# Performance work log

Measured on AMD Instinct MI355X. Metric: run time of the kernel, lower is better.

The kernel has to match this reference:

```python
import jax, jax.numpy as jnp
import numpy as np

BATCH, DIM, HEADS = 512, 2048, 16
CPH = DIM // HEADS  # per-head channels = 128
EPS = 1e-5


def setup_inputs() -> dict:
    key = jax.random.key(0)
    ks = jax.random.split(key, 6)
    x = jax.random.normal(ks[0], (BATCH, DIM, 1, 1), dtype=jnp.float32)
    W_qv = jax.random.normal(ks[1], (2 * DIM, DIM), dtype=jnp.float32) * (1.0 / np.sqrt(DIM))
    temperature = jnp.ones((HEADS, 1, 1), dtype=jnp.float32)
    k_param = jax.random.normal(ks[2], (BATCH, DIM, 1, 1), dtype=jnp.float32)
    bias_param = jax.random.normal(ks[3], (BATCH, HEADS, CPH * CPH, 1), dtype=jnp.float32)
    bn_gamma = jnp.ones((HEADS,), dtype=jnp.float32)
    bn_beta = jnp.zeros((HEADS,), dtype=jnp.float32)
    W_out = jax.random.normal(ks[4], (DIM, DIM, 1, 1), dtype=jnp.float32) * (1.0 / np.sqrt(DIM))
    b_out = jax.random.normal(ks[5], (DIM,), dtype=jnp.float32) * 0.01
    return {"x": x, "W_qv": W_qv, "temperature": temperature, "k_param": k_param,
            "bias_param": bias_param, "bn_gamma": bn_gamma, "bn_beta": bn_beta,
            "W_out": W_out, "b_out": b_out}


def reference(x, W_qv, temperature, k_param, bias_param, bn_gamma, bn_beta, W_out, b_out):
    b, c, h, w = x.shape  # h = w = 1 (required by x.squeeze() + Linear)
    heads = temperature.shape[0]
    cph = c // heads

    xs = x.reshape(b, c)
    qv = xs @ W_qv.T                     # [b, 2c]
    q, v = qv[:, :c], qv[:, c:]
    q = q.reshape(b, heads, cph, 1)      # b head c (h w)
    v = v.reshape(b, heads, cph, 1)
    k = k_param.reshape(b, heads, cph, 1)

    # BatchNorm2d over channel = head (training-mode batch stats, biased var)
    mean = jnp.mean(v, axis=(0, 2, 3), keepdims=True)
    var = jnp.var(v, axis=(0, 2, 3), keepdims=True)
    v = (v - mean) * jax.lax.rsqrt(var + EPS)
    v = v * bn_gamma.reshape(1, heads, 1, 1) + bn_beta.reshape(1, heads, 1, 1)

    # attn = q @ k^T over the singleton spatial dim -> [b, head, cph, cph]
    attn = jnp.einsum('bhcx,bhdx->bhcd', q, k)
    attn = attn + bias_param.reshape(b, heads, cph, cph)
    attn = attn * temperature  # [heads,1,1] broadcasts over batch
    attn = jax.nn.softmax(attn, axis=-1)

    out = jnp.einsum('bhcd,bhdx->bhcx', attn, v)  # [b, head, cph, 1]
    out = out.reshape(b, c)

    # 1x1 conv == matmul
    out = out @ W_out.reshape(c, c).T + b_out
    return out.reshape(b, c, 1, 1)
```

## Files before the change

### kernel.cpp

```cpp
#include <hip/hip_runtime.h>
#include <hip/hip_bf16.h>
#include <cstdint>

#define NBATCH 512
#define NDIM   2048
#define NHEADS 16
#define NCPH   128

typedef __bf16 bf16x8 __attribute__((ext_vector_type(8)));
typedef float  f32x4  __attribute__((ext_vector_type(4)));

__device__ __forceinline__ unsigned short f2bf(float f) {
    uint32_t u = __builtin_bit_cast(uint32_t, f);
    u += 0x7FFFu + ((u >> 16) & 1u);
    return (unsigned short)(u >> 16);
}

__device__ __forceinline__ void gl_lds16(const void* g, void* l) {
    __builtin_amdgcn_global_load_lds(
        (const __attribute__((address_space(1))) void*)g,
        (__attribute__((address_space(3))) void*)l,
        16, 0, 0);
}

template<int BM, int BN, int BK, bool A_BF16, bool BNP>
__global__ __launch_bounds__(256) void gemm_f(
    const unsigned short* __restrict__ Abf, const float* __restrict__ Af,
    const float* __restrict__ Bf, float* __restrict__ C,
    const float* __restrict__ bias, float* __restrict__ bnpart,
    int M, int N, int K)
{
    constexpr int WM = BM / 2, WN = BN / 2;
    constexpr int MI = WM / 16, NI = WN / 16;
    constexpr int CPR = BK / 8;
    constexpr int RA = (BM * BK) / 8 / 256;
    constexpr int GA = (BM * BK) / 2048;
    constexpr int RB = (BN * BK) / 8 / 256;

    __shared__ unsigned short As[2][BM * BK];
    __shared__ unsigned short Bs[2][BN * BK];

    const int tid  = threadIdx.x;
    const int lane = tid & 63;
    const int wid  = tid >> 6;
    const int wr   = wid >> 1;
    const int wc   = wid & 1;
    const int m0   = blockIdx.y * BM;
    const int n0   = blockIdx.x * BN;
    const int fr   = lane & 15;
    const int kq   = lane >> 4;

    f32x4 acc[MI][NI] = {};
    float4 rga[RA > 0 ? RA : 1][2], rgb[RB][2];

    auto load_A = [&](int bs, int k0) {
        if constexpr (A_BF16) {
#pragma unroll
            for (int r = 0; r < GA; r++) {
                const int e   = r * 2048 + tid * 8;
                const int row = e / BK;
                const int swz = ((((e % BK) >> 3) ^ (row & 7)) << 3);
                gl_lds16(Abf + (size_t)(m0 + row) * K + k0 + swz, &As[bs][e]);
            }
        } else {
#pragma unroll
            for (int r = 0; r < RA; r++) {
                const int idx = r * 256 + tid;
                const int row = idx / CPR, cc = idx % CPR;
                const float4* g = (const float4*)(Af + (size_t)(m0 + row) * K
                                                  + k0 + cc * 8);
                rga[r][0] = g[0];
                rga[r][1] = g[1];
            }
        }
    };
    auto load_B = [&](int k0) {
#pragma unroll
        for (int r = 0; r < RB; r++) {
            const int idx = r * 256 + tid;
            const int row = idx / CPR, cc = idx % CPR;
            const float4* g = (const float4*)(Bf + (size_t)(n0 + row) * K
                                              + k0 + cc * 8);
            rgb[r][0] = g[0];
            rgb[r][1] = g[1];
        }
    };
    auto write_A = [&](int bs) {
        if constexpr (!A_BF16) {
#pragma unroll
            for (int r = 0; r < RA; r++) {
                const int idx = r * 256 + tid;
                const int row = idx / CPR, cc = idx % CPR;
                bf16x8 v;
                v[0] = (__bf16)rga[r][0].x; v[1] = (__bf16)rga[r][0].y;
                v[2] = (__bf16)rga[r][0].z; v[3] = (__bf16)rga[r][0].w;
                v[4] = (__bf16)rga[r][1].x; v[5] = (__bf16)rga[r][1].y;
                v[6] = (__bf16)rga[r][1].z; v[7] = (__bf16)rga[r][1].w;
                *(bf16x8*)&As[bs][row * BK + ((cc ^ (row & 7)) << 3)] = v;
            }
        }
    };
    auto write_B = [&](int bs) {
#pragma unroll
        for (int r = 0; r < RB; r++) {
            const int idx = r * 256 + tid;
            const int row = idx / CPR, cc = idx % CPR;
            bf16x8 v;
            v[0] = (__bf16)rgb[r][0].x; v[1] = (__bf16)rgb[r][0].y;
            v[2] = (__bf16)rgb[r][0].z; v[3] = (__bf16)rgb[r][0].w;
            v[4] = (__bf16)rgb[r][1].x; v[5] = (__bf16)rgb[r][1].y;
            v[6] = (__bf16)rgb[r][1].z; v[7] = (__bf16)rgb[r][1].w;
            *(bf16x8*)&Bs[bs][row * BK + ((cc ^ (row & 7)) << 3)] = v;
        }
    };
    auto compute = [&](int bs) {
#pragma unroll
        for (int kh = 0; kh < BK / 32; kh++) {
            const int kchunk = kh * 4 + kq;
            bf16x8 af[MI], bfv[NI];
#pragma unroll
            for (int i = 0; i < MI; i++) {
                const int row = wr * WM + i * 16 + fr;
                af[i] = *(const bf16x8*)&As[bs][row * BK
                        + ((kchunk ^ (row & 7)) << 3)];
            }
#pragma unroll
            for (int j = 0; j < NI; j++) {
                const int row = wc * WN + j * 16 + fr;
                bfv[j] = *(const bf16x8*)&Bs[bs][row * BK
                         + ((kchunk ^ (row & 7)) << 3)];
            }
#pragma unroll
            for (int i = 0; i < MI; i++)
#pragma unroll
                for (int j = 0; j < NI; j++)
                    acc[i][j] = __builtin_amdgcn_mfma_f32_16x16x32_bf16(
                        af[i], bfv[j], acc[i][j], 0, 0, 0);
        }
    };

    load_A(0, 0);
    load_B(0);
    write_A(0);
    write_B(0);
    __syncthreads();

    const int NT = K / BK;
    int cur = 0;
    for (int t = 0; t < NT - 1; t++) {
        load_A(cur ^ 1, (t + 1) * BK);
        load_B((t + 1) * BK);
        compute(cur);
        write_A(cur ^ 1);
        write_B(cur ^ 1);
        __syncthreads();
        cur ^= 1;
    }
    compute(cur);

    const int row0 = m0 + wr * WM + (kq << 2);
    const int col0 = n0 + wc * WN + fr;
#pragma unroll
    for (int j = 0; j < NI; j++) {
        const int cc = col0 + j * 16;
        const float badd = bias ? bias[cc] : 0.0f;
#pragma unroll
        for (int i = 0; i < MI; i++)
#pragma unroll
            for (int r = 0; r < 4; r++)
                C[(size_t)(row0 + i * 16 + r) * N + cc] = acc[i][j][r] + badd;
    }

    if (BNP && n0 >= NDIM) {
        float s = 0.f, ss = 0.f;
#pragma unroll
        for (int i = 0; i < MI; i++)
#pragma unroll
            for (int j = 0; j < NI; j++)
#pragma unroll
                for (int r = 0; r < 4; r++) {
                    const float v = acc[i][j][r];
                    s += v;
                    ss = fmaf(v, v, ss);
                }
#pragma unroll
        for (int off = 32; off; off >>= 1) {
            s  += __shfl_down(s, off);
            ss += __shfl_down(ss, off);
        }
        __shared__ float rs[4], rss[4];
        if (lane == 0) { rs[wid] = s; rss[wid] = ss; }
        __syncthreads();
        if (tid == 0)
            ((float2*)bnpart)[((n0 - NDIM) >> 6) * 8 + (m0 >> 6)] =
                make_float2(rs[0] + rs[1] + rs[2] + rs[3],
                            rss[0] + rss[1] + rss[2] + rss[3]);
    }
}

__global__ __launch_bounds__(256) void attn_k(
    const float* __restrict__ qv, const float* __restrict__ kparam,
    const float* __restrict__ bias, const float* __restrict__ temperature,
    const float* __restrict__ bnpart, const float* __restrict__ gamma,
    const float* __restrict__ beta, unsigned short* __restrict__ aout)
{
    const int bh = blockIdx.x;
    const int b  = bh >> 4;
    const int h  = bh & 15;
    const int tid = threadIdx.x;

    __shared__ float ks[NCPH], vsr[NCPH], s2sh[2];
    if (tid < 32)
        ((float4*)ks)[tid] =
            ((const float4*)(kparam + (size_t)b * NDIM + h * NCPH))[tid];
    else if (tid < 64)
        ((float4*)vsr)[tid - 32] =
            ((const float4*)(qv + (size_t)b * (2 * NDIM) + NDIM + h * NCPH))[tid - 32];

    if (tid < 16) {
        float2 p = ((const float2*)bnpart)[(h * 2 + (tid >> 3)) * 8 + (tid & 7)];
        float s = p.x, ss = p.y;
#pragma unroll
        for (int off = 8; off; off >>= 1) {
            s  += __shfl_xor(s, off);
            ss += __shfl_xor(ss, off);
        }
        if (tid == 0) {
            const float inv = 1.0f / (NBATCH * NCPH);
            float mean = s * inv;
            float var  = ss * inv - mean * mean;
            float sc   = gamma[h] * rsqrtf(var + 1e-5f);
            s2sh[0] = sc;
            s2sh[1] = beta[h] - mean * sc;
        }
    }

    const int c = tid >> 1, half = tid & 1;
    const float qc   = qv[(size_t)b * (2 * NDIM) + h * NCPH + c];
    const float temp = temperature[h];

    const float4* bp = (const float4*)(bias + ((size_t)bh << 14)
                                       + (size_t)c * NCPH + half * 64);
    float4 l4[16];
#pragma unroll
    for (int j = 0; j < 16; j++) l4[j] = bp[j];

    __syncthreads();
    const float sc = s2sh[0], sh = s2sh[1];
    const float4* kk4 = (const float4*)(ks  + half * 64);
    const float4* vv4 = (const float4*)(vsr + half * 64);

    float s0 = 0.f, s1 = 0.f, o0 = 0.f, o1 = 0.f;
#pragma unroll
    for (int j = 0; j < 16; j++) {
        const float4 bb = l4[j];
        const float4 kx = kk4[j];
        const float4 vx = vv4[j];
        float px = __expf(fmaf(qc, kx.x, bb.x) * temp);
        float py = __expf(fmaf(qc, kx.y, bb.y) * temp);
        float pz = __expf(fmaf(qc, kx.z, bb.z) * temp);
        float pw = __expf(fmaf(qc, kx.w, bb.w) * temp);
        s0 += px; s1 += py; s0 += pz; s1 += pw;
        o0 = fmaf(px, vx.x, o0);
        o1 = fmaf(py, vx.y, o1);
        o0 = fmaf(pz, vx.z, o0);
        o1 = fmaf(pw, vx.w, o1);
    }
    float s = s0 + s1, o = o0 + o1;
    s += __shfl_xor(s, 1);
    o += __shfl_xor(o, 1);

    if (half == 0)
        aout[(size_t)b * NDIM + h * NCPH + c] = f2bf(fmaf(sc, o / s, sh));
}

extern "C" void kernel_launch(void* const* d_in, const int* in_sizes, int n_in,
                              void* d_out, int out_size, void* d_ws, size_t ws_size,
                              hipStream_t stream)
{
    const float* x      = (const float*)d_in[0];
    const float* Wqv    = (const float*)d_in[1];
    const float* temp   = (const float*)d_in[2];
    const float* kparam = (const float*)d_in[3];
    const float* bias   = (const float*)d_in[4];
    const float* gamma  = (const float*)d_in[5];
    const float* beta   = (const float*)d_in[6];
    const float* Wout   = (const float*)d_in[7];
    const float* bout   = (const float*)d_in[8];
    float* out = (float*)d_out;

    char* ws = (char*)d_ws;
    float*          qv     = (float*)(ws);
    unsigned short* ao_bf  = (unsigned short*)(ws + 8388608);
    float*          bnpart = (float*)(ws + 10485760);

    gemm_f<64, 64, 128, false, true><<<dim3(64, 8), 256, 0, stream>>>(
        nullptr, x, Wqv, qv, nullptr, bnpart, NBATCH, 2 * NDIM, NDIM);

    attn_k<<<NBATCH * NHEADS, 256, 0, stream>>>(
        qv, kparam, bias, temp, bnpart, gamma, beta, ao_bf);

    gemm_f<64, 32, 128, true, false><<<dim3(64, 8), 256, 0, stream>>>(
        ao_bf, nullptr, Wout, out, bout, nullptr, NBATCH, NDIM, NDIM);
}
```

Measured before the change: 163.1 us.

## Pre-convert Wqv and x to bf16 and stage both QV GEMM operands via direct-to-LDS loads

Adds a conversion kernel that turns W_qv and x into bf16 in workspace on every call. A new GEMM variant then loads both operands with global_load_lds DMA instead of fp32 register loads followed by conversion and LDS writes. The aim is to cut VGPR staging and conversion work in the QV GEMM main loop and let loads overlap compute more cleanly. The cost is an extra kernel launch that reads 32 MB of fp32 and writes 16 MB of bf16, which may outweigh the savings in the GEMM.

Measured after the change: 163.3 us. No clear change (+0.1%).

```diff
diff --git a/kernel.cpp b/kernel.cpp
--- a/kernel.cpp
+++ b/kernel.cpp
@@ -23,19 +23,32 @@
         16, 0, 0);
 }
 
-template<int BM, int BN, int BK, bool A_BF16, bool BNP>
-__global__ __launch_bounds__(256) void gemm_f(
-    const unsigned short* __restrict__ Abf, const float* __restrict__ Af,
-    const float* __restrict__ Bf, float* __restrict__ C,
-    const float* __restrict__ bias, float* __restrict__ bnpart,
+__global__ __launch_bounds__(256) void cvt_wx(
+    const float* __restrict__ wqv, const float* __restrict__ x,
+    unsigned short* __restrict__ owqv, unsigned short* __restrict__ ox)
+{
+    const int t = blockIdx.x * 256 + threadIdx.x;
+    const int n1 = (2 * NDIM * NDIM) / 4;
+    const float4* src; unsigned short* dst; int idx;
+    if (t < n1) { src = (const float4*)wqv; dst = owqv; idx = t; }
+    else        { src = (const float4*)x;   dst = ox;   idx = t - n1; }
+    float4 v = src[idx];
+    ushort4 o;
+    o.x = f2bf(v.x); o.y = f2bf(v.y); o.z = f2bf(v.z); o.w = f2bf(v.w);
+    *(ushort4*)(dst + (size_t)idx * 4) = o;
+}
+
+template<int BM, int BN, int BK, bool BNP>
+__global__ __launch_bounds__(256) void gemm_dma(
+    const unsigned short* __restrict__ Abf,
+    const unsigned short* __restrict__ Bbf,
+    float* __restrict__ C, float* __restrict__ bnpart,
     int M, int N, int K)
 {
     constexpr int WM = BM / 2, WN = BN / 2;
     constexpr int MI = WM / 16, NI = WN / 16;
-    constexpr int CPR = BK / 8;
-    constexpr int RA = (BM * BK) / 8 / 256;
     constexpr int GA = (BM * BK) / 2048;
-    constexpr int RB = (BN * BK) / 8 / 256;
+    constexpr int GB = (BN * BK) / 2048;
 
     __shared__ unsigned short As[2][BM * BK];
     __shared__ unsigned short Bs[2][BN * BK];
@@ -51,27 +64,136 @@
     const int kq   = lane >> 4;
 
     f32x4 acc[MI][NI] = {};
-    float4 rga[RA > 0 ? RA : 1][2], rgb[RB][2];
+
+    auto stage = [&](int bs, int k0) {
+#pragma unroll
+        for (int r = 0; r < GA; r++) {
+            const int e   = r * 2048 + tid * 8;
+            const int row = e / BK;
+            const int swz = ((((e % BK) >> 3) ^ (row & 7)) << 3);
+            gl_lds16(Abf + (size_t)(m0 + row) * K + k0 + swz, &As[bs][e]);
+        }
+#pragma unroll
+        for (int r = 0; r < GB; r++) {
+            const int e   = r * 2048 + tid * 8;
+            const int row = e / BK;
+            const int swz = ((((e % BK) >> 3) ^ (row & 7)) << 3);
+            gl_lds16(Bbf + (size_t)(n0 + row) * K + k0 + swz, &Bs[bs][e]);
+        }
+    };
+    auto compute = [&](int bs) {
+#pragma unroll
+        for (int kh = 0; kh < BK / 32; kh++) {
+            const int kchunk = kh * 4 + kq;
+            bf16x8 af[MI], bfv[NI];
+#pragma unroll
+            for (int i = 0; i < MI; i++) {
+                const int row = wr * WM + i * 16 + fr;
+                af[i] = *(const bf16x8*)&As[bs][row * BK
+                        + ((kchunk ^ (row & 7)) << 3)];
+            }
+#pragma unroll
+            for (int j = 0; j < NI; j++) {
+                const int row = wc * WN + j * 16 + fr;
+                bfv[j] = *(const bf16x8*)&Bs[bs][row * BK
+                         + ((kchunk ^ (row & 7)) << 3)];
+            }
+#pragma unroll
+            for (int i = 0; i < MI; i++)
+#pragma unroll
+                for (int j = 0; j < NI; j++)
+                    acc[i][j] = __builtin_amdgcn_mfma_f32_16x16x32_bf16(
+                        af[i], bfv[j], acc[i][j], 0, 0, 0);
+        }
+    };
+
+    stage(0, 0);
+    __syncthreads();
+
+    const int NT = K / BK;
+    int cur = 0;
+    for (int t = 0; t < NT - 1; t++) {
+        stage(cur ^ 1, (t + 1) * BK);
+        compute(cur);
+        __syncthreads();
+        cur ^= 1;
+    }
+    compute(cur);
+
+    const int row0 = m0 + wr * WM + (kq << 2);
+    const int col0 = n0 + wc * WN + fr;
+#pragma unroll
+    for (int j = 0; j < NI; j++) {
+        const int cc = col0 + j * 16;
+#pragma unroll
+        for (int i = 0; i < MI; i++)
+#pragma unroll
+            for (int r = 0; r < 4; r++)
+                C[(size_t)(row0 + i * 16 + r) * N + cc] = acc[i][j][r];
+    }
+
+    if (BNP && n0 >= NDIM) {
+        float s = 0.f, ss = 0.f;
+#pragma unroll
+        for (int i = 0; i < MI; i++)
+#pragma unroll
+            for (int j = 0; j < NI; j++)
+#pragma unroll
+                for (int r = 0; r < 4; r++) {
+                    const float v = acc[i][j][r];
+                    s += v;
+                    ss = fmaf(v, v, ss);
+                }
+#pragma unroll
+        for (int off = 32; off; off >>= 1) {
+            s  += __shfl_down(s, off);
+            ss += __shfl_down(ss, off);
+        }
+        __shared__ float rs[4], rss[4];
+        if (lane == 0) { rs[wid] = s; rss[wid] = ss; }
+        __syncthreads();
+        if (tid == 0)
+            ((float2*)bnpart)[((n0 - NDIM) >> 6) * 8 + (m0 >> 6)] =
+                make_float2(rs[0] + rs[1] + rs[2] + rs[3],
+                            rss[0] + rss[1] + rss[2] + rss[3]);
+    }
+}
+
+template<int BM, int BN, int BK>
+__global__ __launch_bounds__(256) void gemm_f(
+    const unsigned short* __restrict__ Abf, const float* __restrict__ Bf,
+    float* __restrict__ C, const float* __restrict__ bias,
+    int M, int N, int K)
+{
+    constexpr int WM = BM / 2, WN = BN / 2;
+    constexpr int MI = WM / 16, NI = WN / 16;
+    constexpr int CPR = BK / 8;
+    constexpr int GA = (BM * BK) / 2048;
+    constexpr int RB = (BN * BK) / 8 / 256;
+
+    __shared__ unsigned short As[2][BM * BK];
+    __shared__ unsigned short Bs[2][BN * BK];
+
+    const int tid  = threadIdx.x;
+    const int lane = tid & 63;
+    const int wid  = tid >> 6;
+    const int wr   = wid >> 1;
+    const int wc   = wid & 1;
+    const int m0   = blockIdx.y * BM;
+    const int n0   = blockIdx.x * BN;
+    const int fr   = lane & 15;
+    const int kq   = lane >> 4;
+
+    f32x4 acc[MI][NI] = {};
+    float4 rgb[RB][2];
 
     auto load_A = [&](int bs, int k0) {
-        if constexpr (A_BF16) {
-#pragma unroll
-            for (int r = 0; r < GA; r++) {
-                const int e   = r * 2048 + tid * 8;
-                const int row = e / BK;
-                const int swz = ((((e % BK) >> 3) ^ (row & 7)) << 3);
-                gl_lds16(Abf + (size_t)(m0 + row) * K + k0 + swz, &As[bs][e]);
-            }
-        } else {
-#pragma unroll
-            for (int r = 0; r < RA; r++) {
-                const int idx = r * 256 + tid;
-                const int row = idx / CPR, cc = idx % CPR;
-                const float4* g = (const float4*)(Af + (size_t)(m0 + row) * K
-                                                  + k0 + cc * 8);
-                rga[r][0] = g[0];
-                rga[r][1] = g[1];
-            }
+#pragma unroll
+        for (int r = 0; r < GA; r++) {
+            const int e   = r * 2048 + tid * 8;
+            const int row = e / BK;
+            const int swz = ((((e % BK) >> 3) ^ (row & 7)) << 3);
+            gl_lds16(Abf + (size_t)(m0 + row) * K + k0 + swz, &As[bs][e]);
         }
     };
     auto load_B = [&](int k0) {
@@ -83,21 +205,6 @@
                                               + k0 + cc * 8);
             rgb[r][0] = g[0];
             rgb[r][1] = g[1];
-        }
-    };
-    auto write_A = [&](int bs) {
-        if constexpr (!A_BF16) {
-#pragma unroll
-            for (int r = 0; r < RA; r++) {
-                const int idx = r * 256 + tid;
-                const int row = idx / CPR, cc = idx % CPR;
-                bf16x8 v;
-                v[0] = (__bf16)rga[r][0].x; v[1] = (__bf16)rga[r][0].y;
-                v[2] = (__bf16)rga[r][0].z; v[3] = (__bf16)rga[r][0].w;
-                v[4] = (__bf16)rga[r][1].x; v[5] = (__bf16)rga[r][1].y;
-                v[6] = (__bf16)rga[r][1].z; v[7] = (__bf16)rga[r][1].w;
-                *(bf16x8*)&As[bs][row * BK + ((cc ^ (row & 7)) << 3)] = v;
-            }
         }
     };
     auto write_B = [&](int bs) {
@@ -141,7 +248,6 @@
 
     load_A(0, 0);
     load_B(0);
-    write_A(0);
     write_B(0);
     __syncthreads();
 
@@ -151,7 +257,6 @@
         load_A(cur ^ 1, (t + 1) * BK);
         load_B((t + 1) * BK);
         compute(cur);
-        write_A(cur ^ 1);
         write_B(cur ^ 1);
         __syncthreads();
         cur ^= 1;
@@ -163,38 +268,12 @@
 #pragma unroll
     for (int j = 0; j < NI; j++) {
         const int cc = col0 + j * 16;
-        const float badd = bias ? bias[cc] : 0.0f;
+        const float badd = bias[cc];
 #pragma unroll
         for (int i = 0; i < MI; i++)
 #pragma unroll
             for (int r = 0; r < 4; r++)
                 C[(size_t)(row0 + i * 16 + r) * N + cc] = acc[i][j][r] + badd;
-    }
-
-    if (BNP && n0 >= NDIM) {
-        float s = 0.f, ss = 0.f;
-#pragma unroll
-        for (int i = 0; i < MI; i++)
-#pragma unroll
-            for (int j = 0; j < NI; j++)
-#pragma unroll
-                for (int r = 0; r < 4; r++) {
-                    const float v = acc[i][j][r];
-                    s += v;
-                    ss = fmaf(v, v, ss);
-                }
-#pragma unroll
-        for (int off = 32; off; off >>= 1) {
-            s  += __shfl_down(s, off);
-            ss += __shfl_down(ss, off);
-        }
-        __shared__ float rs[4], rss[4];
-        if (lane == 0) { rs[wid] = s; rss[wid] = ss; }
-        __syncthreads();
-        if (tid == 0)
-            ((float2*)bnpart)[((n0 - NDIM) >> 6) * 8 + (m0 >> 6)] =
-                make_float2(rs[0] + rs[1] + rs[2] + rs[3],
-                            rss[0] + rss[1] + rss[2] + rss[3]);
     }
 }
 
@@ -293,13 +372,17 @@
     float*          qv     = (float*)(ws);
     unsigned short* ao_bf  = (unsigned short*)(ws + 8388608);
     float*          bnpart = (float*)(ws + 10485760);
-
-    gemm_f<64, 64, 128, false, true><<<dim3(64, 8), 256, 0, stream>>>(
-        nullptr, x, Wqv, qv, nullptr, bnpart, NBATCH, 2 * NDIM, NDIM);
+    unsigned short* wqv_bf = (unsigned short*)(ws + 10487808);
+    unsigned short* x_bf   = (unsigned short*)(ws + 27265024);
+
+    cvt_wx<<<9216, 256, 0, stream>>>(Wqv, x, wqv_bf, x_bf);
+
+    gemm_dma<64, 64, 128, true><<<dim3(64, 8), 256, 0, stream>>>(
+        x_bf, wqv_bf, qv, bnpart, NBATCH, 2 * NDIM, NDIM);
 
     attn_k<<<NBATCH * NHEADS, 256, 0, stream>>>(
         qv, kparam, bias, temp, bnpart, gamma, beta, ao_bf);
 
-    gemm_f<64, 32, 128, true, false><<<dim3(64, 8), 256, 0, stream>>>(
-        ao_bf, nullptr, Wout, out, bout, nullptr, NBATCH, NDIM, NDIM);
-}
+    gemm_f<64, 32, 128><<<dim3(64, 8), 256, 0, stream>>>(
+        ao_bf, Wout, out, bout, NBATCH, NDIM, NDIM);
+}
```
